# Kernel tuning notes

Measured on AMD Instinct MI355X. Metric: run time of the kernel, lower is better.

## Reference

```python
import jax, jax.numpy as jnp
import numpy as np

N = 50000
E = 600000
HIDDEN = 128
HEADS = 4
HEAD_DIM = HIDDEN // HEADS
NEG_SLOPE = 0.2
LN_EPS = 1e-5


def setup_inputs() -> dict:
    key = jax.random.key(0)
    ks = jax.random.split(key, 16)
    s = 1.0 / np.sqrt(HIDDEN)
    inp = {
        "h": jax.random.normal(ks[0], (N, HIDDEN), dtype=jnp.float32),
        "src": jax.random.randint(ks[1], (E,), 0, N, dtype=jnp.int32),
        "dst": jax.random.randint(ks[2], (E,), 0, N, dtype=jnp.int32),
        # GATv2 params (share_weights=False, bias=True)
        "W_src": jax.random.normal(ks[3], (HIDDEN, HIDDEN), dtype=jnp.float32) * s,
        "b_src": jnp.zeros((HIDDEN,), dtype=jnp.float32),
        "W_dst": jax.random.normal(ks[4], (HIDDEN, HIDDEN), dtype=jnp.float32) * s,
        "b_dst": jnp.zeros((HIDDEN,), dtype=jnp.float32),
        "attn": jax.random.normal(ks[5], (HEADS, HEAD_DIM), dtype=jnp.float32) * s,
        # FFN params
        "W1": jax.random.normal(ks[6], (HIDDEN, 2 * HIDDEN), dtype=jnp.float32) * s,
        "bf1": jnp.zeros((2 * HIDDEN,), dtype=jnp.float32),
        "W2": jax.random.normal(ks[7], (2 * HIDDEN, HIDDEN), dtype=jnp.float32) * (1.0 / np.sqrt(2 * HIDDEN)),
        "bf2": jnp.zeros((HIDDEN,), dtype=jnp.float32),
        # LayerNorms
        "g1": jnp.ones((HIDDEN,), dtype=jnp.float32),
        "beta1": jnp.zeros((HIDDEN,), dtype=jnp.float32),
        "g2": jnp.ones((HIDDEN,), dtype=jnp.float32),
        "beta2": jnp.zeros((HIDDEN,), dtype=jnp.float32),
    }
    return inp


def _layernorm(x, g, b):
    mu = jnp.mean(x, axis=-1, keepdims=True)
    var = jnp.mean(jnp.square(x - mu), axis=-1, keepdims=True)
    return (x - mu) * jax.lax.rsqrt(var + LN_EPS) * g + b


def reference(h, src, dst, W_src, b_src, W_dst, b_dst, attn,
              W1, bf1, W2, bf2, g1, beta1, g2, beta2):
    # --- GATv2 attention (eval mode, dropouts are identity) ---
    fs = (h @ W_src + b_src).reshape(N, HEADS, HEAD_DIM)   # [N,H,D]
    fd = (h @ W_dst + b_dst).reshape(N, HEADS, HEAD_DIM)
    e = jax.nn.leaky_relu(fs[src] + fd[dst], NEG_SLOPE)    # [E,H,D]
    logits = jnp.einsum('ehd,hd->eh', e, attn)             # [E,H]
    # edge softmax over incoming edges of each dst node
    m = jax.ops.segment_max(logits, dst, num_segments=N)   # [N,H]
    m = jnp.where(jnp.isfinite(m), m, 0.0)                 # guard zero-in-degree
    a = jnp.exp(logits - m[dst])                           # [E,H]
    denom = jax.ops.segment_sum(a, dst, num_segments=N)    # [N,H]
    denom = jnp.where(denom == 0.0, 1.0, denom)
    alpha = a / denom[dst]                                 # [E,H]
    msg = fs[src] * alpha[:, :, None]                      # [E,H,D]
    rst = jax.ops.segment_sum(msg, dst, num_segments=N)    # [N,H,D]
    h_attn = rst.reshape(N, HIDDEN)
    # --- residual + LN, FFN + residual + LN ---
    h1 = _layernorm(h + h_attn, g1, beta1)
    ffn = jax.nn.gelu(h1 @ W1 + bf1, approximate=False) @ W2 + bf2
    out = _layernorm(h1 + ffn, g2, beta2)
    return out
```

## Files before the change

### kernel.cpp

```cpp
#include <hip/hip_runtime.h>
#include <math.h>

#define N_NODES 50000
#define N_EDGES 600000
#define HID 128
#define FFN_HID 256
#define NEG_SLOPE 0.2f
#define LN_EPS 1e-5f
#define BKT 64
#define CSTR 16

typedef unsigned short u16;
typedef unsigned int u32;
typedef __attribute__((ext_vector_type(8))) short short8;
typedef __attribute__((ext_vector_type(4))) float floatx4;

__device__ __forceinline__ u16 f2bf(float x) {
    unsigned int u = __float_as_uint(x);
    unsigned int r = u + 0x7FFFu + ((u >> 16) & 1u);
    return (u16)(r >> 16);
}
__device__ __forceinline__ float bflo(u32 u) { return __uint_as_float(u << 16); }
__device__ __forceinline__ float bfhi(u32 u) { return __uint_as_float(u & 0xffff0000u); }
__device__ __forceinline__ u32 packbf(float lo, float hi) {
    return (u32)f2bf(lo) | ((u32)f2bf(hi) << 16);
}
__device__ __forceinline__ float bf2f(u16 v) { return __uint_as_float(((u32)v) << 16); }
__device__ __forceinline__ float gelu_fast(float v) {
    float u = 1.5957691216057308f * fmaf(0.044715f * v * v, v, v);
    return v / (1.0f + __expf(-u));
}


__global__ __launch_bounds__(256) void scatter_gemm(
    const int* __restrict__ src, const int* __restrict__ dst,
    int* __restrict__ cursor, u16* __restrict__ ebkt,
    const float* __restrict__ h,
    const float* __restrict__ Wsrc, const float* __restrict__ Wdst,
    const float* __restrict__ bsrc, const float* __restrict__ bdst,
    u16* __restrict__ fsb, u16* __restrict__ fdb,
    const float* __restrict__ W1, const float* __restrict__ W2,
    u16* __restrict__ B2sw, u16* __restrict__ B3sw)
{
    __shared__ u16 bs[4][16][64 * 8];
    int bid = blockIdx.x;
    if (bid >= 1610) {
        int t0 = (bid - 1610) * 256 + threadIdx.x;
        {
            int n = t0 & 255, k = t0 >> 8;
            int frag = (n >> 4) * 4 + (k >> 5);
            int lane = ((k >> 3) & 3) * 16 + (n & 15);
            int j = k & 7;
            B2sw[((size_t)frag * 64 + lane) * 8 + j] = f2bf(W1[(size_t)k * FFN_HID + n]);
        }
        {
            int n = t0 & 127, k = t0 >> 7;
            int frag = (n >> 4) * 8 + (k >> 5);
            int lane = ((k >> 3) & 3) * 16 + (n & 15);
            int j = k & 7;
            B3sw[((size_t)frag * 64 + lane) * 8 + j] = f2bf(W2[(size_t)k * HID + n]);
        }
        return;
    }
    bool isGemm = (bid < 1536) && ((bid % 3) != 2);
    if (!isGemm) {
        int sid = (bid < 1536) ? (bid / 3) : (512 + bid - 1536);
        int t4 = sid * 256 + threadIdx.x;
        if (t4 < N_EDGES / 4) {
            uint4 d4 = *(const uint4*)&dst[t4 * 4];
            uint4 s4 = *(const uint4*)&src[t4 * 4];
            int slot0 = atomicAdd(&cursor[(int)d4.x * CSTR], 1);
            int slot1 = atomicAdd(&cursor[(int)d4.y * CSTR], 1);
            int slot2 = atomicAdd(&cursor[(int)d4.z * CSTR], 1);
            int slot3 = atomicAdd(&cursor[(int)d4.w * CSTR], 1);
            if (slot0 < BKT) ebkt[(size_t)d4.x * BKT + slot0] = (u16)s4.x;
            if (slot1 < BKT) ebkt[(size_t)d4.y * BKT + slot1] = (u16)s4.y;
            if (slot2 < BKT) ebkt[(size_t)d4.z * BKT + slot2] = (u16)s4.z;
            if (slot3 < BKT) ebkt[(size_t)d4.w * BKT + slot3] = (u16)s4.w;
        }
        return;
    }
    int gid = (bid / 3) * 2 + (bid % 3);
    int tid = threadIdx.x, wave = tid >> 6, lane = tid & 63;
    int lrow = lane & 15, lq = lane >> 4;
    float bias[4];
    #pragma unroll
    for (int nt = 0; nt < 4; nt++) {
        int cg = wave * 64 + nt * 16 + lrow;
        const float* Wp = (cg < HID) ? (Wsrc + cg) : (Wdst + cg - HID);
        bias[nt] = (cg < HID) ? bsrc[cg] : bdst[cg - HID];
        #pragma unroll
        for (int ks = 0; ks < 4; ks++) {
            short8 b;
            #pragma unroll
            for (int j = 0; j < 8; j++)
                b[j] = (short)f2bf(Wp[(size_t)(ks * 32 + lq * 8 + j) * HID]);
            *(short8*)&bs[wave][nt * 4 + ks][lane * 8] = b;
        }
    }
    for (int mb = gid; mb < N_NODES / 16; mb += 1024) {
        int m0 = mb * 16;
        const float* hrow = h + (size_t)(m0 + lrow) * HID;
        floatx4 acc[4];
        #pragma unroll
        for (int nt = 0; nt < 4; nt++) acc[nt] = {0.f, 0.f, 0.f, 0.f};
        #pragma unroll
        for (int ks = 0; ks < 4; ks++) {
            float4 va = *(const float4*)(hrow + ks * 32 + lq * 8);
            float4 vb = *(const float4*)(hrow + ks * 32 + lq * 8 + 4);
            short8 a;
            a[0] = (short)f2bf(va.x); a[1] = (short)f2bf(va.y);
            a[2] = (short)f2bf(va.z); a[3] = (short)f2bf(va.w);
            a[4] = (short)f2bf(vb.x); a[5] = (short)f2bf(vb.y);
            a[6] = (short)f2bf(vb.z); a[7] = (short)f2bf(vb.w);
            #pragma unroll
            for (int nt = 0; nt < 4; nt++) {
                short8 b = *(const short8*)&bs[wave][nt * 4 + ks][lane * 8];
                acc[nt] = __builtin_amdgcn_mfma_f32_16x16x32_bf16(a, b, acc[nt], 0, 0, 0);
            }
        }
        #pragma unroll
        for (int nt = 0; nt < 4; nt++) {
            int cg = wave * 64 + nt * 16 + lrow;
            u16* outp = (cg < HID) ? fsb : fdb;
            int c = cg & (HID - 1);
            #pragma unroll
            for (int r = 0; r < 4; r++) {
                int row = m0 + lq * 4 + r;
                outp[(size_t)row * HID + c] = f2bf(acc[nt][r] + bias[nt]);
            }
        }
    }
}


__global__ __launch_bounds__(256) void aggregate_kernel(
    const u16* __restrict__ fsb, const u16* __restrict__ fdb,
    const float* __restrict__ h, const float* __restrict__ attn,
    const int* __restrict__ cursor, const u16* __restrict__ ebkt,
    const float* __restrict__ g1, const float* __restrict__ beta1,
    u16* __restrict__ h1b)
{
    int wave = threadIdx.x >> 6, lane = threadIdx.x & 63;
    int node = blockIdx.x * 4 + wave;
    if (node >= N_NODES) return;
    int grp = lane >> 4, fl = lane & 15;
    int f = fl * 8;

    uint4 ud = *(const uint4*)&fdb[(size_t)node * HID + f];
    float fdv[8] = { bflo(ud.x), bfhi(ud.x), bflo(ud.y), bfhi(ud.y),
                     bflo(ud.z), bfhi(ud.z), bflo(ud.w), bfhi(ud.w) };
    float4 aA = *(const float4*)&attn[f];
    float4 aB = *(const float4*)&attn[f + 4];
    float c1[8] = { 0.6f * aA.x, 0.6f * aA.y, 0.6f * aA.z, 0.6f * aA.w,
                    0.6f * aB.x, 0.6f * aB.y, 0.6f * aB.z, 0.6f * aB.w };
    float c2[8] = { 0.4f * aA.x, 0.4f * aA.y, 0.4f * aA.z, 0.4f * aA.w,
                    0.4f * aB.x, 0.4f * aB.y, 0.4f * aB.z, 0.4f * aB.w };

    int cnt = cursor[node * CSTR]; cnt = cnt < BKT ? cnt : BKT;
    const u16* brow = ebkt + (size_t)node * BKT;
    float acc[8] = {0.f, 0.f, 0.f, 0.f, 0.f, 0.f, 0.f, 0.f};
    float lsum = 0.f;

    auto loadrow = [&](int e) -> uint4 {
        int s = (int)brow[e];
        return *(const uint4*)&fsb[(size_t)s * HID + f];
    };
    auto compute = [&](uint4 u) {
        float x[8] = { bflo(u.x), bfhi(u.x), bflo(u.y), bfhi(u.y),
                       bflo(u.z), bfhi(u.z), bflo(u.w), bfhi(u.w) };
        float p = 0.f;
        #pragma unroll
        for (int i = 0; i < 8; i++) {
            float ei = x[i] + fdv[i];
            p = fmaf(c1[i], ei, p);
            p = fmaf(c2[i], fabsf(ei), p);
        }
        p += __shfl_xor(p, 1); p += __shfl_xor(p, 2);
        float w = __expf(p);
        lsum += w;
        #pragma unroll
        for (int i = 0; i < 8; i++) acc[i] = fmaf(w, x[i], acc[i]);
    };

    {
        int e = grp;
        uint4 bufA, bufB;
        bool vA = (e < cnt), vB = (e + 4 < cnt);
        if (vA) bufA = loadrow(e);
        if (vB) bufB = loadrow(e + 4);
        while (vA) {
            int en = e + 8;
            uint4 bufC; bool vC = (en < cnt);
            if (vC) bufC = loadrow(en);
            compute(bufA);
            bufA = bufB; vA = vB;
            bufB = bufC; vB = vC;
            e += 4;
        }
    }

    #pragma unroll
    for (int i = 0; i < 8; i++) {
        acc[i] += __shfl_xor(acc[i], 16);
        acc[i] += __shfl_xor(acc[i], 32);
    }
    lsum += __shfl_xor(lsum, 16); lsum += __shfl_xor(lsum, 32);

    float inv = (lsum > 0.f) ? (1.0f / lsum) : 0.f;
    float4 h0 = *(const float4*)&h[(size_t)node * HID + f];
    float4 h1v = *(const float4*)&h[(size_t)node * HID + f + 4];
    float hx[8] = { h0.x, h0.y, h0.z, h0.w, h1v.x, h1v.y, h1v.z, h1v.w };
    float o[8], s1 = 0.f, s2 = 0.f;
    #pragma unroll
    for (int i = 0; i < 8; i++) {
        o[i] = hx[i] + acc[i] * inv;
        s1 += o[i]; s2 += o[i] * o[i];
    }
    s1 += __shfl_xor(s1, 1); s2 += __shfl_xor(s2, 1);
    s1 += __shfl_xor(s1, 2); s2 += __shfl_xor(s2, 2);
    s1 += __shfl_xor(s1, 4); s2 += __shfl_xor(s2, 4);
    s1 += __shfl_xor(s1, 8); s2 += __shfl_xor(s2, 8);
    float mu = s1 * (1.0f / HID);
    float var = s2 * (1.0f / HID) - mu * mu;
    float rs = rsqrtf(var + LN_EPS);
    if (grp == 0) {
        float4 gA = *(const float4*)&g1[f], gB = *(const float4*)&g1[f + 4];
        float4 bA = *(const float4*)&beta1[f], bB = *(const float4*)&beta1[f + 4];
        float q0 = (o[0] - mu) * rs * gA.x + bA.x, q1 = (o[1] - mu) * rs * gA.y + bA.y;
        float q2 = (o[2] - mu) * rs * gA.z + bA.z, q3 = (o[3] - mu) * rs * gA.w + bA.w;
        float q4 = (o[4] - mu) * rs * gB.x + bB.x, q5 = (o[5] - mu) * rs * gB.y + bB.y;
        float q6 = (o[6] - mu) * rs * gB.z + bB.z, q7 = (o[7] - mu) * rs * gB.w + bB.w;
        uint4 ob;
        ob.x = packbf(q0, q1); ob.y = packbf(q2, q3);
        ob.z = packbf(q4, q5); ob.w = packbf(q6, q7);
        *(uint4*)&h1b[(size_t)node * HID + f] = ob;
    }
}


#define TS_PAD 8

__global__ __launch_bounds__(256) void ffn_fused(
    const u16* __restrict__ h1b,
    const u16* __restrict__ B2sw, const u16* __restrict__ B3sw,
    const float* __restrict__ bf1, const float* __restrict__ bf2,
    const float* __restrict__ g2, const float* __restrict__ beta2,
    float* __restrict__ out)
{
    __shared__ u16 ts[16][FFN_HID + TS_PAD];
    __shared__ float xs[16][HID];
    int tid = threadIdx.x, wave = tid >> 6, lane = tid & 63;
    int lrow = lane & 15, lq = lane >> 4;

    short8 b1f[4][4];
    #pragma unroll
    for (int nt = 0; nt < 4; nt++)
        #pragma unroll
        for (int ks = 0; ks < 4; ks++) {
            int frag = (wave * 4 + nt) * 4 + ks;
            b1f[nt][ks] = *(const short8*)(B2sw + ((size_t)frag * 64 + lane) * 8);
        }
    short8 b2f[2][8];
    #pragma unroll
    for (int nt = 0; nt < 2; nt++)
        #pragma unroll
        for (int ks = 0; ks < 8; ks++) {
            int frag = (wave * 2 + nt) * 8 + ks;
            b2f[nt][ks] = *(const short8*)(B3sw + ((size_t)frag * 64 + lane) * 8);
        }
    float bias1[4];
    #pragma unroll
    for (int nt = 0; nt < 4; nt++) bias1[nt] = bf1[wave * 64 + nt * 16 + lrow];
    float bias2[2];
    #pragma unroll
    for (int nt = 0; nt < 2; nt++) bias2[nt] = bf2[wave * 32 + nt * 16 + lrow];

    for (int mb = blockIdx.x; mb < N_NODES / 16; mb += gridDim.x) {
        int m0 = mb * 16;
        floatx4 acc1[4];
        #pragma unroll
        for (int nt = 0; nt < 4; nt++) acc1[nt] = {0.f, 0.f, 0.f, 0.f};
        #pragma unroll
        for (int ks = 0; ks < 4; ks++) {
            short8 a = *(const short8*)(h1b + (size_t)(m0 + lrow) * HID + ks * 32 + lq * 8);
            #pragma unroll
            for (int nt = 0; nt < 4; nt++)
                acc1[nt] = __builtin_amdgcn_mfma_f32_16x16x32_bf16(a, b1f[nt][ks], acc1[nt], 0, 0, 0);
        }
        #pragma unroll
        for (int nt = 0; nt < 4; nt++) {
            int cg = wave * 64 + nt * 16 + lrow;
            #pragma unroll
            for (int r = 0; r < 4; r++) {
                float v = acc1[nt][r] + bias1[nt];
                ts[lq * 4 + r][cg] = f2bf(gelu_fast(v));
            }
        }
        __syncthreads();
        floatx4 acc2[2];
        #pragma unroll
        for (int nt = 0; nt < 2; nt++) acc2[nt] = {0.f, 0.f, 0.f, 0.f};
        #pragma unroll
        for (int ks = 0; ks < 8; ks++) {
            short8 a = *(const short8*)&ts[lrow][ks * 32 + lq * 8];
            #pragma unroll
            for (int nt = 0; nt < 2; nt++)
                acc2[nt] = __builtin_amdgcn_mfma_f32_16x16x32_bf16(a, b2f[nt][ks], acc2[nt], 0, 0, 0);
        }
        #pragma unroll
        for (int nt = 0; nt < 2; nt++) {
            int cg = wave * 32 + nt * 16 + lrow;
            #pragma unroll
            for (int r = 0; r < 4; r++) {
                int row = m0 + lq * 4 + r;
                float resid = bf2f(h1b[(size_t)row * HID + cg]);
                xs[lq * 4 + r][cg] = acc2[nt][r] + bias2[nt] + resid;
            }
        }
        __syncthreads();
        int row = tid >> 4, c0 = (tid & 15) * 8;
        float v[8];
        float s1 = 0.f, s2 = 0.f;
        #pragma unroll
        for (int i = 0; i < 8; i++) { v[i] = xs[row][c0 + i]; s1 += v[i]; s2 += v[i] * v[i]; }
        s1 += __shfl_xor(s1, 1); s2 += __shfl_xor(s2, 1);
        s1 += __shfl_xor(s1, 2); s2 += __shfl_xor(s2, 2);
        s1 += __shfl_xor(s1, 4); s2 += __shfl_xor(s2, 4);
        s1 += __shfl_xor(s1, 8); s2 += __shfl_xor(s2, 8);
        float mu = s1 * (1.0f / HID);
        float var = s2 * (1.0f / HID) - mu * mu;
        float rs = rsqrtf(var + LN_EPS);
        float o[8];
        #pragma unroll
        for (int i = 0; i < 8; i++) o[i] = (v[i] - mu) * rs * g2[c0 + i] + beta2[c0 + i];
        float* op = out + (size_t)(m0 + row) * HID + c0;
        *(float4*)(op)     = make_float4(o[0], o[1], o[2], o[3]);
        *(float4*)(op + 4) = make_float4(o[4], o[5], o[6], o[7]);
        __syncthreads();
    }
}


extern "C" void kernel_launch(void* const* d_in, const int* in_sizes, int n_in,
                              void* d_out, int out_size, void* d_ws, size_t ws_size,
                              hipStream_t stream)
{
    const float* h    = (const float*)d_in[0];
    const int*   src  = (const int*)d_in[1];
    const int*   dst  = (const int*)d_in[2];
    const float* Wsrc = (const float*)d_in[3];
    const float* bsrc = (const float*)d_in[4];
    const float* Wdst = (const float*)d_in[5];
    const float* bdst = (const float*)d_in[6];
    const float* attn = (const float*)d_in[7];
    const float* W1   = (const float*)d_in[8];
    const float* bf1  = (const float*)d_in[9];
    const float* W2   = (const float*)d_in[10];
    const float* bf2  = (const float*)d_in[11];
    const float* g1   = (const float*)d_in[12];
    const float* beta1= (const float*)d_in[13];
    const float* g2   = (const float*)d_in[14];
    const float* beta2= (const float*)d_in[15];
    float* out = (float*)d_out;

    u16* fsb = (u16*)d_ws;
    u16* fdb = fsb + (size_t)N_NODES * HID;
    u16* h1b = fdb + (size_t)N_NODES * HID;
    u16* B2 = h1b + (size_t)N_NODES * HID;
    u16* B3 = B2 + 32768;
    int* cursor = (int*)(B3 + 32768);
    u16* ebkt   = (u16*)(cursor + (size_t)N_NODES * CSTR);

    hipMemsetAsync(cursor, 0, (size_t)N_NODES * CSTR * sizeof(int), stream);
    scatter_gemm<<<1738, 256, 0, stream>>>(src, dst, cursor, ebkt,
                                           h, Wsrc, Wdst, bsrc, bdst, fsb, fdb,
                                           W1, W2, B2, B3);
    aggregate_kernel<<<(N_NODES + 3) / 4, 256, 0, stream>>>(fsb, fdb, h, attn, cursor, ebkt, g1, beta1, h1b);
    ffn_fused<<<640, 256, 0, stream>>>(h1b, B2, B3, bf1, bf2, g2, beta2, out);
}
```

Measured before the change: 213.2 us.

## Partition edge scatter by dst residue so each block handles one node class

Scatter blocks are regrouped so that eight blocks share a chunk of edges, and each block only inserts edges whose dst node index mod 8 equals its partition id. This is meant to localize the atomic cursor updates and bucket writes to a subset of nodes per block, presumably to improve cache or channel locality of the scattered atomics. In exchange, every block now reads eight times as many src/dst entries and evaluates a filter per edge, and the grid shrinks by two blocks to match the new chunking.

Result: slower. 234.8 us (+10.2%).

```diff
diff --git a/kernel.cpp b/kernel.cpp
--- a/kernel.cpp
+++ b/kernel.cpp
@@ -31,6 +31,8 @@
     return v / (1.0f + __expf(-u));
 }
 
+
+#define ECHUNK 2055
 
 __global__ __launch_bounds__(256) void scatter_gemm(
     const int* __restrict__ src, const int* __restrict__ dst,
@@ -44,8 +46,8 @@
 {
     __shared__ u16 bs[4][16][64 * 8];
     int bid = blockIdx.x;
-    if (bid >= 1610) {
-        int t0 = (bid - 1610) * 256 + threadIdx.x;
+    if (bid >= 1608) {
+        int t0 = (bid - 1608) * 256 + threadIdx.x;
         {
             int n = t0 & 255, k = t0 >> 8;
             int frag = (n >> 4) * 4 + (k >> 5);
@@ -64,19 +66,30 @@
     }
     bool isGemm = (bid < 1536) && ((bid % 3) != 2);
     if (!isGemm) {
-        int sid = (bid < 1536) ? (bid / 3) : (512 + bid - 1536);
-        int t4 = sid * 256 + threadIdx.x;
-        if (t4 < N_EDGES / 4) {
+        int p = bid & 7;
+        int chunk = (bid < 1536) ? ((bid / 3) >> 3) : (64 + ((bid - 1536) >> 3));
+        int e4beg = chunk * ECHUNK;
+        int e4end = (chunk + 1) * ECHUNK;
+        if (e4end > N_EDGES / 4) e4end = N_EDGES / 4;
+        for (int t4 = e4beg + threadIdx.x; t4 < e4end; t4 += 256) {
             uint4 d4 = *(const uint4*)&dst[t4 * 4];
             uint4 s4 = *(const uint4*)&src[t4 * 4];
-            int slot0 = atomicAdd(&cursor[(int)d4.x * CSTR], 1);
-            int slot1 = atomicAdd(&cursor[(int)d4.y * CSTR], 1);
-            int slot2 = atomicAdd(&cursor[(int)d4.z * CSTR], 1);
-            int slot3 = atomicAdd(&cursor[(int)d4.w * CSTR], 1);
-            if (slot0 < BKT) ebkt[(size_t)d4.x * BKT + slot0] = (u16)s4.x;
-            if (slot1 < BKT) ebkt[(size_t)d4.y * BKT + slot1] = (u16)s4.y;
-            if (slot2 < BKT) ebkt[(size_t)d4.z * BKT + slot2] = (u16)s4.z;
-            if (slot3 < BKT) ebkt[(size_t)d4.w * BKT + slot3] = (u16)s4.w;
+            if ((int)(d4.x & 7) == p) {
+                int slot = atomicAdd(&cursor[(int)d4.x * CSTR], 1);
+                if (slot < BKT) ebkt[(size_t)d4.x * BKT + slot] = (u16)s4.x;
+            }
+            if ((int)(d4.y & 7) == p) {
+                int slot = atomicAdd(&cursor[(int)d4.y * CSTR], 1);
+                if (slot < BKT) ebkt[(size_t)d4.y * BKT + slot] = (u16)s4.y;
+            }
+            if ((int)(d4.z & 7) == p) {
+                int slot = atomicAdd(&cursor[(int)d4.z * CSTR], 1);
+                if (slot < BKT) ebkt[(size_t)d4.z * BKT + slot] = (u16)s4.z;
+            }
+            if ((int)(d4.w & 7) == p) {
+                int slot = atomicAdd(&cursor[(int)d4.w * CSTR], 1);
+                if (slot < BKT) ebkt[(size_t)d4.w * BKT + slot] = (u16)s4.w;
+            }
         }
         return;
     }
@@ -373,7 +386,7 @@
     u16* ebkt   = (u16*)(cursor + (size_t)N_NODES * CSTR);
 
     hipMemsetAsync(cursor, 0, (size_t)N_NODES * CSTR * sizeof(int), stream);
-    scatter_gemm<<<1738, 256, 0, stream>>>(src, dst, cursor, ebkt,
+    scatter_gemm<<<1736, 256, 0, stream>>>(src, dst, cursor, ebkt,
                                            h, Wsrc, Wdst, bsrc, bdst, fsb, fdb,
                                            W1, W2, B2, B3);
     aggregate_kernel<<<(N_NODES + 3) / 4, 256, 0, stream>>>(fsb, fdb, h, attn, cursor, ebkt, g1, beta1, h1b);
```
